# Performance work log

Measured on AMD Instinct MI355X. Metric: run time of the kernel, lower is better.

The kernel has to match this reference:

```python
import jax, jax.numpy as jnp
import numpy as np

# H36M-style 17-joint skeleton: bones[b] = (parent_joint, child_joint)
BONES = [(0,1),(1,2),(2,3),(0,4),(4,5),(5,6),(0,7),(7,8),(8,9),(9,10),
         (8,11),(11,12),(12,13),(8,14),(14,15),(15,16)]
N_JOINTS = 17
ROOT = 0


def _euler_xyz_to_matrix(e):
    # pytorch3d euler_angles_to_matrix(e, 'XYZ'): R = Rx(a) @ Ry(b) @ Rz(c)
    cx, cy, cz = jnp.cos(e[..., 0]), jnp.cos(e[..., 1]), jnp.cos(e[..., 2])
    sx, sy, sz = jnp.sin(e[..., 0]), jnp.sin(e[..., 1]), jnp.sin(e[..., 2])
    one, zero = jnp.ones_like(cx), jnp.zeros_like(cx)
    shp = e.shape[:-1] + (3, 3)
    Rx = jnp.stack([one, zero, zero, zero, cx, -sx, zero, sx, cx], -1).reshape(shp)
    Ry = jnp.stack([cy, zero, sy, zero, one, zero, -sy, zero, cy], -1).reshape(shp)
    Rz = jnp.stack([cz, -sz, zero, sz, cz, zero, zero, zero, one], -1).reshape(shp)
    return Rx @ Ry @ Rz


def setup_inputs() -> dict:
    key = jax.random.key(0)
    k1, k2 = jax.random.split(key)
    N = 500000
    euler_angle = jax.random.normal(k1, (N, 16, 3), dtype=jnp.float32)
    bone_length = jax.random.uniform(k2, (N, 16, 1), dtype=jnp.float32)
    return {"euler_angle": euler_angle, "bone_length": bone_length}


def reference(euler_angle, bone_length):
    # euler_angle: (N, 16, 3), bone_length: (N, 16, 1)
    N = euler_angle.shape[0]
    R = _euler_xyz_to_matrix(euler_angle)  # (N, 16, 3, 3)
    # Accumulated rotations in pytorch3d row-vector convention: p' = p @ M,
    # compose(M_parent, R_i) -> M_parent @ R_i.
    M = [None] * N_JOINTS
    pos = [None] * N_JOINTS
    M[ROOT] = jnp.broadcast_to(jnp.eye(3, dtype=euler_angle.dtype), (N, 3, 3))
    pos[ROOT] = jnp.zeros((N, 3), dtype=euler_angle.dtype)
    for i, (j0, j1) in enumerate(BONES):
        M[j1] = jnp.einsum('nij,njk->nik', M[j0], R[:, i])
        # local offset is (0, 0, L) so p @ M == L * M[:, 2, :] (third row)
        pos[j1] = bone_length[:, i, 0, None] * M[j1][:, 2, :] + pos[j0]
    return jnp.stack(pos, axis=1)  # (N, 17, 3)
```

## Files before the change

### kernel.cpp

```cpp
#include <hip/hip_runtime.h>


#define NB 128

__device__ __forceinline__ void mm3(const float A[9], const float B[9], float C[9]) {
#pragma unroll
    for (int r = 0; r < 3; ++r) {
        C[3*r+0] = A[3*r+0]*B[0] + A[3*r+1]*B[3] + A[3*r+2]*B[6];
        C[3*r+1] = A[3*r+0]*B[1] + A[3*r+1]*B[4] + A[3*r+2]*B[7];
        C[3*r+2] = A[3*r+0]*B[2] + A[3*r+1]*B[5] + A[3*r+2]*B[8];
    }
}

__device__ __forceinline__ void euler_rot(const float* __restrict__ ev, int i, float R[9]) {
    float a = ev[3*i+0], b = ev[3*i+1], c = ev[3*i+2];
    float sx, cx, sy, cy, sz, cz;
    __sincosf(a, &sx, &cx);
    __sincosf(b, &sy, &cy);
    __sincosf(c, &sz, &cz);
    R[0] = cy*cz;             R[1] = -cy*sz;            R[2] = sy;
    R[3] = sx*sy*cz + cx*sz;  R[4] = -sx*sy*sz + cx*cz; R[5] = -sx*cy;
    R[6] = -cx*sy*cz + sx*sz; R[7] = cx*sy*sz + sx*cz;  R[8] = cx*cy;
}

__global__ void __launch_bounds__(NB)
fk17_kernel(const float* __restrict__ euler, const float* __restrict__ blen,
            float* __restrict__ out, int n)
{
    __shared__ float s_o[NB * 51];

    const int tid    = threadIdx.x;
    const int block0 = blockIdx.x * NB;
    const int nvalid = min(NB, n - block0);
    const int t      = block0 + tid;

    if (tid < nvalid) {
        float ev[48];
        const float4* ge4 = (const float4*)(euler + (size_t)t * 48);
#pragma unroll
        for (int q = 0; q < 12; ++q) {
            float4 v = ge4[q];
            ev[4*q+0] = v.x; ev[4*q+1] = v.y; ev[4*q+2] = v.z; ev[4*q+3] = v.w;
        }
        float L[16];
        const float4* gb4 = (const float4*)(blen + (size_t)t * 16);
#pragma unroll
        for (int q = 0; q < 4; ++q) {
            float4 v = gb4[q];
            L[4*q+0] = v.x; L[4*q+1] = v.y; L[4*q+2] = v.z; L[4*q+3] = v.w;
        }

        float* o = s_o + tid * 51;
        float Ma[9], Mb[9], M8[9], R[9];
        float px, py, pz, p8x, p8y, p8z;

        o[0] = 0.f; o[1] = 0.f; o[2] = 0.f;

        euler_rot(ev, 0, Ma);
        px = L[0]*Ma[6]; py = L[0]*Ma[7]; pz = L[0]*Ma[8];
        o[3] = px; o[4] = py; o[5] = pz;
        euler_rot(ev, 1, R); mm3(Ma, R, Mb);
        px += L[1]*Mb[6]; py += L[1]*Mb[7]; pz += L[1]*Mb[8];
        o[6] = px; o[7] = py; o[8] = pz;
        euler_rot(ev, 2, R); mm3(Mb, R, Ma);
        px += L[2]*Ma[6]; py += L[2]*Ma[7]; pz += L[2]*Ma[8];
        o[9] = px; o[10] = py; o[11] = pz;

        euler_rot(ev, 3, Ma);
        px = L[3]*Ma[6]; py = L[3]*Ma[7]; pz = L[3]*Ma[8];
        o[12] = px; o[13] = py; o[14] = pz;
        euler_rot(ev, 4, R); mm3(Ma, R, Mb);
        px += L[4]*Mb[6]; py += L[4]*Mb[7]; pz += L[4]*Mb[8];
        o[15] = px; o[16] = py; o[17] = pz;
        euler_rot(ev, 5, R); mm3(Mb, R, Ma);
        px += L[5]*Ma[6]; py += L[5]*Ma[7]; pz += L[5]*Ma[8];
        o[18] = px; o[19] = py; o[20] = pz;

        euler_rot(ev, 6, Ma);
        px = L[6]*Ma[6]; py = L[6]*Ma[7]; pz = L[6]*Ma[8];
        o[21] = px; o[22] = py; o[23] = pz;
        euler_rot(ev, 7, R); mm3(Ma, R, M8);
        px += L[7]*M8[6]; py += L[7]*M8[7]; pz += L[7]*M8[8];
        o[24] = px; o[25] = py; o[26] = pz;
        p8x = px; p8y = py; p8z = pz;

        euler_rot(ev, 8, R); mm3(M8, R, Ma);
        px = p8x + L[8]*Ma[6]; py = p8y + L[8]*Ma[7]; pz = p8z + L[8]*Ma[8];
        o[27] = px; o[28] = py; o[29] = pz;
        euler_rot(ev, 9, R); mm3(Ma, R, Mb);
        px += L[9]*Mb[6]; py += L[9]*Mb[7]; pz += L[9]*Mb[8];
        o[30] = px; o[31] = py; o[32] = pz;

        euler_rot(ev, 10, R); mm3(M8, R, Ma);
        px = p8x + L[10]*Ma[6]; py = p8y + L[10]*Ma[7]; pz = p8z + L[10]*Ma[8];
        o[33] = px; o[34] = py; o[35] = pz;
        euler_rot(ev, 11, R); mm3(Ma, R, Mb);
        px += L[11]*Mb[6]; py += L[11]*Mb[7]; pz += L[11]*Mb[8];
        o[36] = px; o[37] = py; o[38] = pz;
        euler_rot(ev, 12, R); mm3(Mb, R, Ma);
        px += L[12]*Ma[6]; py += L[12]*Ma[7]; pz += L[12]*Ma[8];
        o[39] = px; o[40] = py; o[41] = pz;

        euler_rot(ev, 13, R); mm3(M8, R, Ma);
        px = p8x + L[13]*Ma[6]; py = p8y + L[13]*Ma[7]; pz = p8z + L[13]*Ma[8];
        o[42] = px; o[43] = py; o[44] = pz;
        euler_rot(ev, 14, R); mm3(Ma, R, Mb);
        px += L[14]*Mb[6]; py += L[14]*Mb[7]; pz += L[14]*Mb[8];
        o[45] = px; o[46] = py; o[47] = pz;
        euler_rot(ev, 15, R); mm3(Mb, R, Ma);
        px += L[15]*Ma[6]; py += L[15]*Ma[7]; pz += L[15]*Ma[8];
        o[48] = px; o[49] = py; o[50] = pz;
    }
    __syncthreads();

    float* og = out + (size_t)block0 * 51;
    if (nvalid == NB) {
        const float4* so4 = (const float4*)s_o;
        float4*       og4 = (float4*)og;
        for (int i4 = tid; i4 < NB * 51 / 4; i4 += NB)
            og4[i4] = so4[i4];
    } else {
        const int tot = nvalid * 51;
        for (int i = tid; i < tot; i += NB)
            og[i] = s_o[i];
    }
}

extern "C" void kernel_launch(void* const* d_in, const int* in_sizes, int n_in,
                              void* d_out, int out_size, void* d_ws, size_t ws_size,
                              hipStream_t stream) {
    const float* euler = (const float*)d_in[0];
    const float* blen  = (const float*)d_in[1];
    float* out = (float*)d_out;

    const int n    = in_sizes[0] / 48;
    const int grid = (n + NB - 1) / NB;
    fk17_kernel<<<grid, NB, 0, stream>>>(euler, blen, out, n);
}
```

Before: 201.9 us.

## Split output staging into two halves to shrink shared memory per block

Computation is split into two phases: joints 0-8 are written to a 27-float-per-thread shared buffer and flushed to global, then joints 9-16 reuse the same buffer and are flushed. This roughly halves LDS per block to allow more resident blocks per CU. In exchange, the float4 vectorized coalesced copy becomes scalar strided stores with integer division, plus extra barriers, and ev/L/M8 stay live across the sync, raising register pressure.

```diff
diff --git a/kernel.cpp b/kernel.cpp
--- a/kernel.cpp
+++ b/kernel.cpp
@@ -2,6 +2,8 @@
 
 
 #define NB 128
+#define CA 27
+#define CB 24
 
 __device__ __forceinline__ void mm3(const float A[9], const float B[9], float C[9]) {
 #pragma unroll
@@ -27,32 +29,35 @@
 fk17_kernel(const float* __restrict__ euler, const float* __restrict__ blen,
             float* __restrict__ out, int n)
 {
-    __shared__ float s_o[NB * 51];
+    __shared__ float s_o[NB * CA];
 
     const int tid    = threadIdx.x;
     const int block0 = blockIdx.x * NB;
     const int nvalid = min(NB, n - block0);
     const int t      = block0 + tid;
 
+    float ev[48];
+    float L[16];
+    float M8[9];
+    float p8x, p8y, p8z;
+
     if (tid < nvalid) {
-        float ev[48];
         const float4* ge4 = (const float4*)(euler + (size_t)t * 48);
+        const float4* gb4 = (const float4*)(blen + (size_t)t * 16);
 #pragma unroll
         for (int q = 0; q < 12; ++q) {
             float4 v = ge4[q];
             ev[4*q+0] = v.x; ev[4*q+1] = v.y; ev[4*q+2] = v.z; ev[4*q+3] = v.w;
         }
-        float L[16];
-        const float4* gb4 = (const float4*)(blen + (size_t)t * 16);
 #pragma unroll
         for (int q = 0; q < 4; ++q) {
             float4 v = gb4[q];
             L[4*q+0] = v.x; L[4*q+1] = v.y; L[4*q+2] = v.z; L[4*q+3] = v.w;
         }
 
-        float* o = s_o + tid * 51;
-        float Ma[9], Mb[9], M8[9], R[9];
-        float px, py, pz, p8x, p8y, p8z;
+        float* o = s_o + tid * CA;
+        float Ma[9], Mb[9], R[9];
+        float px, py, pz;
 
         o[0] = 0.f; o[1] = 0.f; o[2] = 0.f;
 
@@ -83,46 +88,62 @@
         px += L[7]*M8[6]; py += L[7]*M8[7]; pz += L[7]*M8[8];
         o[24] = px; o[25] = py; o[26] = pz;
         p8x = px; p8y = py; p8z = pz;
+    }
+    __syncthreads();
+
+    {
+        float* og = out + (size_t)block0 * 51;
+        const int tot = nvalid * CA;
+        for (int i = tid; i < tot; i += NB) {
+            int s = i / CA;
+            int j = i - s * CA;
+            og[s * 51 + j] = s_o[i];
+        }
+    }
+    __syncthreads();
+
+    if (tid < nvalid) {
+        float* o = s_o + tid * CA;
+        float Ma[9], Mb[9], R[9];
+        float px, py, pz;
 
         euler_rot(ev, 8, R); mm3(M8, R, Ma);
         px = p8x + L[8]*Ma[6]; py = p8y + L[8]*Ma[7]; pz = p8z + L[8]*Ma[8];
-        o[27] = px; o[28] = py; o[29] = pz;
+        o[0] = px; o[1] = py; o[2] = pz;
         euler_rot(ev, 9, R); mm3(Ma, R, Mb);
         px += L[9]*Mb[6]; py += L[9]*Mb[7]; pz += L[9]*Mb[8];
-        o[30] = px; o[31] = py; o[32] = pz;
+        o[3] = px; o[4] = py; o[5] = pz;
 
         euler_rot(ev, 10, R); mm3(M8, R, Ma);
         px = p8x + L[10]*Ma[6]; py = p8y + L[10]*Ma[7]; pz = p8z + L[10]*Ma[8];
-        o[33] = px; o[34] = py; o[35] = pz;
+        o[6] = px; o[7] = py; o[8] = pz;
         euler_rot(ev, 11, R); mm3(Ma, R, Mb);
         px += L[11]*Mb[6]; py += L[11]*Mb[7]; pz += L[11]*Mb[8];
-        o[36] = px; o[37] = py; o[38] = pz;
+        o[9] = px; o[10] = py; o[11] = pz;
         euler_rot(ev, 12, R); mm3(Mb, R, Ma);
         px += L[12]*Ma[6]; py += L[12]*Ma[7]; pz += L[12]*Ma[8];
-        o[39] = px; o[40] = py; o[41] = pz;
+        o[12] = px; o[13] = py; o[14] = pz;
 
         euler_rot(ev, 13, R); mm3(M8, R, Ma);
         px = p8x + L[13]*Ma[6]; py = p8y + L[13]*Ma[7]; pz = p8z + L[13]*Ma[8];
-        o[42] = px; o[43] = py; o[44] = pz;
+        o[15] = px; o[16] = py; o[17] = pz;
         euler_rot(ev, 14, R); mm3(Ma, R, Mb);
         px += L[14]*Mb[6]; py += L[14]*Mb[7]; pz += L[14]*Mb[8];
-        o[45] = px; o[46] = py; o[47] = pz;
+        o[18] = px; o[19] = py; o[20] = pz;
         euler_rot(ev, 15, R); mm3(Mb, R, Ma);
         px += L[15]*Ma[6]; py += L[15]*Ma[7]; pz += L[15]*Ma[8];
-        o[48] = px; o[49] = py; o[50] = pz;
+        o[21] = px; o[22] = py; o[23] = pz;
     }
     __syncthreads();
 
-    float* og = out + (size_t)block0 * 51;
-    if (nvalid == NB) {
-        const float4* so4 = (const float4*)s_o;
-        float4*       og4 = (float4*)og;
-        for (int i4 = tid; i4 < NB * 51 / 4; i4 += NB)
-            og4[i4] = so4[i4];
-    } else {
-        const int tot = nvalid * 51;
-        for (int i = tid; i < tot; i += NB)
-            og[i] = s_o[i];
+    {
+        float* og = out + (size_t)block0 * 51 + CA;
+        const int tot = nvalid * CB;
+        for (int i = tid; i < tot; i += NB) {
+            int s = i / CB;
+            int j = i - s * CB;
+            og[s * 51 + j] = s_o[s * CA + j];
+        }
     }
 }
 
```

Result: slower. 248.3 us (+23.0%).
